# Optimization experiments

Measured on AMD Instinct MI355X. Metric: run time of the kernel, lower is better.

The kernel has to match this reference:

```python
import jax, jax.numpy as jnp
import numpy as np


def _depthwise3x3(x_nhwc, w):
    # w: (3, 3, 1, C) — depthwise conv, padding=1, matches torch Conv2d(groups=C)
    return jax.lax.conv_general_dilated(
        x_nhwc, w, window_strides=(1, 1), padding='SAME',
        dimension_numbers=('NHWC', 'HWIO', 'NHWC'),
        feature_group_count=x_nhwc.shape[-1])


def _stripe_attn(q, k, v, lepe_w, B, H, W, nh, hd, ss, axis, scale):
    # q/k/v: (B, H, W, nh*hd); axis 0 = horizontal stripes, 1 = vertical
    pad_h = (-H) % ss if axis == 0 else 0
    pad_w = (-W) % ss if axis == 1 else 0
    if pad_h or pad_w:
        pad = ((0, 0), (0, pad_h), (0, pad_w), (0, 0))
        q, k, v = jnp.pad(q, pad), jnp.pad(k, pad), jnp.pad(v, pad)
    Hp, Wp = q.shape[1], q.shape[2]
    lepe = _depthwise3x3(v, lepe_w)  # (B, Hp, Wp, nh*hd)

    if axis == 0:
        nS = Hp // ss
        def to_win(t):  # -> (B*nS*Wp, nh, ss, hd)
            t = t.reshape(B, nS, ss, Wp, nh, hd)
            return t.transpose(0, 1, 3, 4, 2, 5).reshape(B * nS * Wp, nh, ss, hd)
    else:
        nS = Wp // ss
        def to_win(t):  # -> (B*Hp*nS, nh, ss, hd)
            t = t.reshape(B, Hp, nS, ss, nh, hd)
            return t.transpose(0, 1, 2, 4, 3, 5).reshape(B * Hp * nS, nh, ss, hd)

    qw, kw, vw, lw = to_win(q), to_win(k), to_win(v), to_win(lepe)
    attn = jax.nn.softmax(jnp.einsum('wnqd,wnkd->wnqk', qw, kw) / scale, axis=-1)
    out = jnp.einsum('wnqk,wnkd->wnqd', attn, vw) + lw  # (Wnum, nh, ss, hd)

    if axis == 0:
        out = out.transpose(0, 2, 1, 3).reshape(B, nS, Wp, ss, nh * hd)
        out = out.transpose(0, 1, 3, 2, 4).reshape(B, Hp, Wp, nh * hd)
    else:
        out = out.transpose(0, 2, 1, 3).reshape(B, Hp, nS, ss, nh * hd)
        out = out.reshape(B, Hp, Wp, nh * hd)
    return out[:, :H, :W, :].reshape(B, H * W, nh * hd)


def setup_inputs() -> dict:
    key = jax.random.key(0)
    ks = jax.random.split(key, 6)
    B, H, W, dim, n_heads, ss = 8, 64, 64, 512, 16, 8
    half = dim // 2
    x = jax.random.normal(ks[0], (B, H * W, dim), dtype=jnp.float32)
    w_qkv = jax.random.normal(ks[1], (3 * dim, dim), dtype=jnp.float32) * 0.02
    w_proj = jax.random.normal(ks[2], (dim, dim), dtype=jnp.float32) * 0.02
    b_proj = jnp.zeros((dim,), dtype=jnp.float32)
    lepe_h_w = jax.random.normal(ks[3], (3, 3, 1, half), dtype=jnp.float32) * 0.1
    lepe_v_w = jax.random.normal(ks[4], (3, 3, 1, half), dtype=jnp.float32) * 0.1
    return {"x": x, "w_qkv": w_qkv, "w_proj": w_proj, "b_proj": b_proj,
            "lepe_h_w": lepe_h_w, "lepe_v_w": lepe_v_w, "H": H, "W": W}


def reference(x, w_qkv, w_proj, b_proj, lepe_h_w, lepe_v_w, H, W):
    B, L, C = x.shape
    n_heads, ss = 16, 8
    hd = C // n_heads
    scale = float(np.sqrt(hd))
    qkv = x @ w_qkv.T  # (B, L, 3C)
    q, k, v = jnp.split(qkv, 3, axis=-1)
    q = q.reshape(B, H, W, C)
    k = k.reshape(B, H, W, C)
    v = v.reshape(B, H, W, C)
    half = C // 2
    nh_h = n_heads // 2
    nh_v = n_heads - nh_h
    out_h = _stripe_attn(q[..., :half], k[..., :half], v[..., :half],
                         lepe_h_w, B, H, W, nh_h, hd, ss, axis=0, scale=scale)
    out_v = _stripe_attn(q[..., half:], k[..., half:], v[..., half:],
                         lepe_v_w, B, H, W, nh_v, hd, ss, axis=1, scale=scale)
    out = jnp.concatenate([out_h, out_v], axis=-1)
    return out @ w_proj.T + b_proj
```

## Files before the change

### kernel.cpp

```cpp
#include <hip/hip_runtime.h>
#include <hip/hip_bf16.h>
#include <stdint.h>

typedef _Float16 half2v __attribute__((ext_vector_type(2)));
typedef _Float16 half8v __attribute__((ext_vector_type(8)));
typedef uint32_t u32x4  __attribute__((ext_vector_type(4)));
typedef float    f32x4  __attribute__((ext_vector_type(4)));

__device__ __forceinline__ unsigned short f2h(float f) {
  _Float16 h = (_Float16)f;
  return __builtin_bit_cast(unsigned short, h);
}
__device__ __forceinline__ half2v bch2(uint32_t u) {
  return __builtin_bit_cast(half2v, u);
}
__device__ __forceinline__ uint32_t pkrtz_u32(float a, float b) {
  return __builtin_bit_cast(uint32_t, __builtin_amdgcn_cvt_pkrtz(a, b));
}

__device__ __forceinline__ int qkv_idx(int half, int b, int n, int h, int w) {
  int idx = half * 8388608 + (b * 8 + n) * 131072;
  idx += (half == 0) ? ((h >> 3) * 16384 + w * 256 + (h & 7) * 32)
                     : (h * 2048 + w * 32);
  return idx;
}

#define GLOAD_LDS16(gsrc, lbase)                                          \
  __builtin_amdgcn_global_load_lds(                                       \
      (const __attribute__((address_space(1))) uint32_t*)(gsrc),          \
      (__attribute__((address_space(3))) uint32_t*)(lbase), 16, 0, 0)

__global__ __launch_bounds__(256) void cvt_f32_f16(const float* __restrict__ in,
                                                   unsigned short* __restrict__ out,
                                                   int n4) {
  int i = blockIdx.x * 256 + threadIdx.x;
  if (i >= n4) return;
  float4 f = reinterpret_cast<const float4*>(in)[i];
  ushort4 u;
  u.x = f2h(f.x); u.y = f2h(f.y); u.z = f2h(f.z); u.w = f2h(f.w);
  reinterpret_cast<ushort4*>(out)[i] = u;
}

template<int MODE>
__global__ __launch_bounds__(512, 2) void gemm8(
    const unsigned short* __restrict__ A,
    const unsigned short* __restrict__ Bm,
    unsigned short* __restrict__ Cq,
    float* __restrict__ Cf,
    const float* __restrict__ bias,
    int M, int N)
{
  constexpr int K = 512;
  constexpr int NIT = 4;
  __shared__ unsigned short As[2][256 * 64];
  __shared__ unsigned short Bs[2][256 * 64];
  const int tid  = threadIdx.x;
  const int gn   = N >> 8;
  const int cpx  = gridDim.x >> 3;
  const int bid  = blockIdx.x;
  const int wgid = (bid & 7) * cpx + (bid >> 3);
  const int m0   = (wgid / gn) * 256;
  const int n0   = (wgid % gn) * 256;
  const int wave = tid >> 6, lane = tid & 63;
  const int wr  = wave >> 2;
  const int wcn = wave & 3;

  const int srow = tid >> 3;
  const int schk = ((tid & 7) ^ (srow & 7)) * 8;
  const size_t aSrc = (size_t)(m0 + srow) * K + schk;
  const size_t bSrc = (size_t)(n0 + srow) * K + schk;
  char* ldsA = (char*)(&As[0][0]) + (tid & ~63) * 16;
  char* ldsB = (char*)(&Bs[0][0]) + (tid & ~63) * 16;

#define STAGE_A8(b, kt)                                                     \
  do {                                                                      \
    GLOAD_LDS16(A + aSrc + (size_t)(kt) * 64,             ldsA + (b) * 32768);         \
    GLOAD_LDS16(A + aSrc + (size_t)64 * K + (kt) * 64,    ldsA + (b) * 32768 + 8192);  \
    GLOAD_LDS16(A + aSrc + (size_t)128 * K + (kt) * 64,   ldsA + (b) * 32768 + 16384); \
    GLOAD_LDS16(A + aSrc + (size_t)192 * K + (kt) * 64,   ldsA + (b) * 32768 + 24576); \
  } while (0)
#define STAGE_B8(b, kt)                                                     \
  do {                                                                      \
    GLOAD_LDS16(Bm + bSrc + (size_t)(kt) * 64,            ldsB + (b) * 32768);         \
    GLOAD_LDS16(Bm + bSrc + (size_t)64 * K + (kt) * 64,   ldsB + (b) * 32768 + 8192);  \
    GLOAD_LDS16(Bm + bSrc + (size_t)128 * K + (kt) * 64,  ldsB + (b) * 32768 + 16384); \
    GLOAD_LDS16(Bm + bSrc + (size_t)192 * K + (kt) * 64,  ldsB + (b) * 32768 + 24576); \
  } while (0)
#define BARS                                                                \
  __builtin_amdgcn_s_barrier();                                             \
  __builtin_amdgcn_sched_barrier(0)

  STAGE_A8(0, 0);
  STAGE_B8(0, 0);
  STAGE_B8(1, 1);

  f32x4 acc[8][4];
  const f32x4 zero = {0.f, 0.f, 0.f, 0.f};
  #pragma unroll
  for (int i = 0; i < 8; ++i)
    #pragma unroll
    for (int j = 0; j < 4; ++j) acc[i][j] = zero;

  const int lr  = lane & 15;
  const int kg  = lane >> 4;
  const int ck0 = kg ^ (lr & 7);

  asm volatile("s_waitcnt vmcnt(4)" ::: "memory");
  BARS;

#define LD_AF(buf, mg, ks)                                                  \
  do {                                                                      \
    const unsigned short* ap = &As[buf][0] +                                \
        (wr * 128 + (mg) * 64 + lr) * 64 + (((ks) ? (ck0 ^ 4) : ck0)) * 8;  \
    af[0] = *(const half8v*)(ap);                                           \
    af[1] = *(const half8v*)(ap + 1024);                                    \
    af[2] = *(const half8v*)(ap + 2048);                                    \
    af[3] = *(const half8v*)(ap + 3072);                                    \
  } while (0)
#define LD_BF(buf, ks)                                                      \
  do {                                                                      \
    const unsigned short* bp = &Bs[buf][0] +                                \
        (wcn * 64 + lr) * 64 + (((ks) ? (ck0 ^ 4) : ck0)) * 8;              \
    bf[0] = *(const half8v*)(bp);                                           \
    bf[1] = *(const half8v*)(bp + 1024);                                    \
    bf[2] = *(const half8v*)(bp + 2048);                                    \
    bf[3] = *(const half8v*)(bp + 3072);                                    \
  } while (0)
#define MROW(mg, i)                                                         \
  acc[(mg)*4+(i)][0] = __builtin_amdgcn_mfma_f32_16x16x32_f16(bf[0], af[i], acc[(mg)*4+(i)][0], 0, 0, 0); \
  acc[(mg)*4+(i)][1] = __builtin_amdgcn_mfma_f32_16x16x32_f16(bf[1], af[i], acc[(mg)*4+(i)][1], 0, 0, 0); \
  acc[(mg)*4+(i)][2] = __builtin_amdgcn_mfma_f32_16x16x32_f16(bf[2], af[i], acc[(mg)*4+(i)][2], 0, 0, 0); \
  acc[(mg)*4+(i)][3] = __builtin_amdgcn_mfma_f32_16x16x32_f16(bf[3], af[i], acc[(mg)*4+(i)][3], 0, 0, 0);
#define MFMA16(mg)                                                          \
  do {                                                                      \
    __builtin_amdgcn_s_setprio(1);                                          \
    MROW(mg, 0); MROW(mg, 1); MROW(mg, 2); MROW(mg, 3);                     \
    __builtin_amdgcn_s_setprio(0);                                          \
  } while (0)

  for (int it2 = 0; it2 < NIT; ++it2) {
    const bool more = (it2 + 1 < NIT);
    const int keven = 2 * it2;
    half8v af[4], bf[4];
    LD_BF(0, 0); LD_AF(0, 0, 0);
    STAGE_A8(1, keven + 1);
    BARS;
    MFMA16(0);
    BARS;
    LD_AF(0, 1, 0);
    BARS;
    MFMA16(1);
    BARS;
    LD_BF(0, 1); LD_AF(0, 0, 1);
    BARS;
    MFMA16(0);
    BARS;
    LD_AF(0, 1, 1);
    if (more) {
      STAGE_B8(0, keven + 2);
      asm volatile("s_waitcnt vmcnt(4)" ::: "memory");
    } else {
      asm volatile("s_waitcnt vmcnt(0)" ::: "memory");
    }
    BARS;
    MFMA16(1);
    BARS;
    LD_BF(1, 0); LD_AF(1, 0, 0);
    if (more) STAGE_A8(0, keven + 2);
    BARS;
    MFMA16(0);
    BARS;
    LD_AF(1, 1, 0);
    BARS;
    MFMA16(1);
    BARS;
    LD_BF(1, 1); LD_AF(1, 0, 1);
    BARS;
    MFMA16(0);
    BARS;
    LD_AF(1, 1, 1);
    if (more) {
      STAGE_B8(1, keven + 3);
      asm volatile("s_waitcnt vmcnt(4)" ::: "memory");
    }
    BARS;
    MFMA16(1);
    BARS;
  }
#undef STAGE_A8
#undef STAGE_B8
#undef LD_AF
#undef LD_BF
#undef MROW
#undef MFMA16
#undef BARS

  const int cr = (lane >> 4) * 4;
  const int cc = lane & 15;

  if constexpr (MODE == 0) {
    #pragma unroll
    for (int j = 0; j < 4; ++j) {
      const int n = n0 + wcn * 64 + j * 16 + cr;
      const float4 b4 = *reinterpret_cast<const float4*>(bias + n);
      #pragma unroll
      for (int i = 0; i < 8; ++i) {
        const int m = m0 + wr * 128 + i * 16 + cc;
        float4 r;
        r.x = acc[i][j][0] + b4.x;
        r.y = acc[i][j][1] + b4.y;
        r.z = acc[i][j][2] + b4.z;
        r.w = acc[i][j][3] + b4.w;
        *reinterpret_cast<float4*>(Cf + (size_t)m * N + n) = r;
      }
    }
  } else {
    const int mb   = m0 + wr * 128;
    const int btok = mb >> 12;
    const int hr0  = (mb >> 6) & 63;
    #pragma unroll
    for (int j = 0; j < 4; ++j) {
      const int nb    = n0 + wcn * 64 + j * 16 + cr;
      const int tq    = nb >> 9;
      const int halfc = (nb >> 8) & 1;
      const int nn    = (nb & 255) >> 5;
      const int ch4   = nb & 31;
      const int headbase = tq * 16777216 + halfc * 8388608 +
                           (btok * 8 + nn) * 131072 + ch4;
      #pragma unroll
      for (int i = 0; i < 8; ++i) {
        const int hrow = hr0 + (i >> 2);
        const int wpix = (i & 3) * 16 + cc;
        const int off = halfc ? (hrow * 2048 + wpix * 32)
                              : ((hrow >> 3) * 16384 + wpix * 256 + (hrow & 7) * 32);
        uint2 r;
        r.x = pkrtz_u32(acc[i][j][0], acc[i][j][1]);
        r.y = pkrtz_u32(acc[i][j][2], acc[i][j][3]);
        *reinterpret_cast<uint2*>(Cq + headbase + off) = r;
      }
    }
  }
}

__global__ __launch_bounds__(256) void attn_lepe(
    const unsigned short* __restrict__ qkvp,
    const unsigned short* __restrict__ wlep,
    unsigned short* __restrict__ outp)
{
  const int gw   = (int)((blockIdx.x * 256 + threadIdx.x) >> 6);
  const int lane = threadIdx.x & 63;
  const int half = gw >> 14;
  const int id   = gw & 16383;
  const int b    = id >> 11;
  const int n    = (id >> 8) & 7;
  int h0, w0;
  if (half == 0) { h0 = ((id >> 5) & 7) * 8; w0 = (id & 31) * 2; }
  else           { h0 = ((id >> 3) & 31) * 2; w0 = (id & 7) * 8; }
  const int baseA = qkv_idx(half, b, n, h0, w0);
  const int dWin  = (half == 0) ? 256 : 2048;
  const int baseB = baseA + dWin;

  const int qr = lane >> 3, kr = lane & 7;
  const unsigned short* qA = qkvp + baseA + qr * 32;
  const unsigned short* kA = qkvp + 16777216 + baseA + kr * 32;
  float sA = 0.f, sB = 0.f;
  #pragma unroll
  for (int c = 0; c < 4; ++c) {
    const u32x4 qa = *reinterpret_cast<const u32x4*>(qA + c * 8);
    const u32x4 ka = *reinterpret_cast<const u32x4*>(kA + c * 8);
    const u32x4 qb = *reinterpret_cast<const u32x4*>(qA + dWin + c * 8);
    const u32x4 kb = *reinterpret_cast<const u32x4*>(kA + dWin + c * 8);
    #pragma unroll
    for (int e = 0; e < 4; ++e) {
      sA = __builtin_amdgcn_fdot2(bch2(qa[e]), bch2(ka[e]), sA, false);
      sB = __builtin_amdgcn_fdot2(bch2(qb[e]), bch2(kb[e]), sB, false);
    }
  }
  const float scl = 0.17677669529663687f;
  const float pA = __expf(sA * scl);
  const float pB = __expf(sB * scl);
  float denA = pA, denB = pB;
  denA += __shfl_xor(denA, 1); denA += __shfl_xor(denA, 2); denA += __shfl_xor(denA, 4);
  denB += __shfl_xor(denB, 1); denB += __shfl_xor(denB, 2); denB += __shfl_xor(denB, 4);
  const float aAv = pA * __builtin_amdgcn_rcpf(denA);
  const float aBv = pB * __builtin_amdgcn_rcpf(denB);
  const uint32_t adu = pkrtz_u32(aAv, aBv);

  const int dgrp = lane & 3;
  const int win  = (lane >> 2) & 1;
  const int qr2  = lane >> 3;
  const int d0   = dgrp * 8;
  const int mybase = win ? baseB : baseA;
  const unsigned short* vwin = qkvp + 33554432 + mybase;

  half2v o01 = {0,0}, o23 = {0,0}, o45 = {0,0}, o67 = {0,0};
  #pragma unroll
  for (int k = 0; k < 8; ++k) {
    const uint32_t pairw = (uint32_t)__shfl((int)adu, qr2 * 8 + k);
    const half2v ph = bch2(pairw);
    const _Float16 av = win ? ph.y : ph.x;
    const half2v ak2 = {av, av};
    const u32x4 vv = *reinterpret_cast<const u32x4*>(vwin + k * 32 + d0);
    o01 += ak2 * bch2(vv[0]);
    o23 += ak2 * bch2(vv[1]);
    o45 += ak2 * bch2(vv[2]);
    o67 += ak2 * bch2(vv[3]);
  }

  const int hq = (half == 0) ? (h0 + qr2) : (h0 + win);
  const int wq = (half == 0) ? (w0 + win) : (w0 + qr2);
  const unsigned short* vplane = qkvp + 33554432;
  const unsigned short* wl = wlep + half * 2304 + n * 32 + d0;
  half2v l01 = {0,0}, l23 = {0,0}, l45 = {0,0}, l67 = {0,0};
  #pragma unroll
  for (int dy = -1; dy <= 1; ++dy) {
    #pragma unroll
    for (int dx = -1; dx <= 1; ++dx) {
      const int hh = hq + dy, ww = wq + dx;
      u32x4 vv = {0u, 0u, 0u, 0u};
      if ((unsigned)hh < 64u && (unsigned)ww < 64u)
        vv = *reinterpret_cast<const u32x4*>(vplane + qkv_idx(half, b, n, hh, ww) + d0);
      const u32x4 wt = *reinterpret_cast<const u32x4*>(wl + ((dy + 1) * 3 + dx + 1) * 256);
      l01 += bch2(wt[0]) * bch2(vv[0]);
      l23 += bch2(wt[1]) * bch2(vv[1]);
      l45 += bch2(wt[2]) * bch2(vv[2]);
      l67 += bch2(wt[3]) * bch2(vv[3]);
    }
  }

  const int m = b * 4096 + hq * 64 + wq;
  const int chan0 = half * 256 + n * 32;
  u32x4 r;
  r[0] = __builtin_bit_cast(uint32_t, (half2v)(o01 + l01));
  r[1] = __builtin_bit_cast(uint32_t, (half2v)(o23 + l23));
  r[2] = __builtin_bit_cast(uint32_t, (half2v)(o45 + l45));
  r[3] = __builtin_bit_cast(uint32_t, (half2v)(o67 + l67));
  *reinterpret_cast<u32x4*>(outp + (size_t)m * 512 + chan0 + d0) = r;
}

extern "C" void kernel_launch(void* const* d_in, const int* in_sizes, int n_in,
                              void* d_out, int out_size, void* d_ws, size_t ws_size,
                              hipStream_t stream) {
  const float* x      = (const float*)d_in[0];
  const float* w_qkv  = (const float*)d_in[1];
  const float* w_proj = (const float*)d_in[2];
  const float* b_proj = (const float*)d_in[3];
  const float* lepe_h = (const float*)d_in[4];
  const float* lepe_v = (const float*)d_in[5];
  float* out = (float*)d_out;

  char* ws = (char*)d_ws;
  unsigned short* qkv_p   = (unsigned short*)ws;
  unsigned short* xh      = (unsigned short*)(ws + 100663296);
  unsigned short* wqkv_h  = (unsigned short*)(ws + 134217728);
  unsigned short* wproj_h = (unsigned short*)(ws + 135790592);
  unsigned short* wlep_h  = (unsigned short*)(ws + 136314880);

  cvt_f32_f16<<<16384, 256, 0, stream>>>(x, xh, 4194304);
  cvt_f32_f16<<<768,   256, 0, stream>>>(w_qkv, wqkv_h, 196608);
  cvt_f32_f16<<<256,   256, 0, stream>>>(w_proj, wproj_h, 65536);
  cvt_f32_f16<<<3,     256, 0, stream>>>(lepe_h, wlep_h, 576);
  cvt_f32_f16<<<3,     256, 0, stream>>>(lepe_v, wlep_h + 2304, 576);

  gemm8<1><<<768, 512, 0, stream>>>(
      xh, wqkv_h, qkv_p, nullptr, nullptr, 32768, 1536);

  attn_lepe<<<8192, 256, 0, stream>>>(qkv_p, wlep_h, xh);

  gemm8<0><<<256, 512, 0, stream>>>(
      xh, wproj_h, nullptr, out, b_proj, 32768, 512);
}
```

Before: 175.6 us.

## Add smaller-tile projection GEMM and merge weight conversion launches

The final projection GEMM (M=32768, N=512) moves from the 256x256-tile gemm8 with 256 blocks to a new 128x128-tile kernel with 1024 blocks of 256 threads. The aim is better fill of the GPU's compute units, which the few large tiles left underused. The four small weight-conversion launches are also merged into one kernel to cut launch overhead. The cost is lower data reuse per tile and more global traffic for A and B.

```diff
diff --git a/kernel.cpp b/kernel.cpp
--- a/kernel.cpp
+++ b/kernel.cpp
@@ -39,6 +39,25 @@
   ushort4 u;
   u.x = f2h(f.x); u.y = f2h(f.y); u.z = f2h(f.z); u.w = f2h(f.w);
   reinterpret_cast<ushort4*>(out)[i] = u;
+}
+
+__global__ __launch_bounds__(256) void cvt_weights(
+    const float* __restrict__ wqkv, const float* __restrict__ wproj,
+    const float* __restrict__ lh,   const float* __restrict__ lv,
+    unsigned short* __restrict__ owqkv, unsigned short* __restrict__ owproj,
+    unsigned short* __restrict__ owlep)
+{
+  int i = blockIdx.x * 256 + threadIdx.x;
+  const float* src; unsigned short* dst; int off;
+  if      (i < 196608) { src = wqkv;  dst = owqkv;        off = i; }
+  else if (i < 262144) { src = wproj; dst = owproj;       off = i - 196608; }
+  else if (i < 262720) { src = lh;    dst = owlep;        off = i - 262144; }
+  else if (i < 263296) { src = lv;    dst = owlep + 2304; off = i - 262720; }
+  else return;
+  float4 f = reinterpret_cast<const float4*>(src)[off];
+  ushort4 u;
+  u.x = f2h(f.x); u.y = f2h(f.y); u.z = f2h(f.z); u.w = f2h(f.w);
+  reinterpret_cast<ushort4*>(dst)[off] = u;
 }
 
 template<int MODE>
@@ -242,6 +261,105 @@
   }
 }
 
+__global__ __launch_bounds__(256) void gemm_proj(
+    const unsigned short* __restrict__ A,
+    const unsigned short* __restrict__ B,
+    float* __restrict__ Cf,
+    const float* __restrict__ bias)
+{
+  constexpr int K = 512, N = 512;
+  __shared__ unsigned short As[2][128 * 32];
+  __shared__ unsigned short Bs[2][128 * 32];
+  const int tid  = threadIdx.x;
+  const int gn   = N >> 7;
+  const int cpx  = gridDim.x >> 3;
+  const int bid  = blockIdx.x;
+  const int wgid = (bid & 7) * cpx + (bid >> 3);
+  const int m0   = (wgid / gn) * 128;
+  const int n0   = (wgid % gn) * 128;
+  const int wave = tid >> 6, lane = tid & 63;
+  const int wr = wave >> 1, wc = wave & 1;
+  const int sr = tid >> 2;
+  const int sc = ((tid & 3) ^ ((tid >> 3) & 3)) * 8;
+  const size_t aBase0 = (size_t)(m0 + sr) * K + sc;
+  const size_t aBase1 = (size_t)(m0 + 64 + sr) * K + sc;
+  const size_t bBase0 = (size_t)(n0 + sr) * K + sc;
+  const size_t bBase1 = (size_t)(n0 + 64 + sr) * K + sc;
+  char* ldsA = (char*)(&As[0][0]) + (tid & ~63) * 16;
+  char* ldsB = (char*)(&Bs[0][0]) + (tid & ~63) * 16;
+
+#define STAGE_P(bsel, kofs)                                        \
+  do {                                                             \
+    GLOAD_LDS16(A + aBase0 + (kofs), ldsA + (bsel) * 8192);        \
+    GLOAD_LDS16(A + aBase1 + (kofs), ldsA + (bsel) * 8192 + 4096); \
+    GLOAD_LDS16(B + bBase0 + (kofs), ldsB + (bsel) * 8192);        \
+    GLOAD_LDS16(B + bBase1 + (kofs), ldsB + (bsel) * 8192 + 4096); \
+  } while (0)
+
+  STAGE_P(0, 0);
+
+  f32x4 acc[4][4];
+  const f32x4 zero = {0.f, 0.f, 0.f, 0.f};
+  #pragma unroll
+  for (int i = 0; i < 4; ++i)
+    #pragma unroll
+    for (int j = 0; j < 4; ++j) acc[i][j] = zero;
+
+  const int lr   = lane & 15;
+  const int slot = (lane >> 4) ^ ((lr >> 1) & 3);
+
+  auto compute = [&](const unsigned short* Asb, const unsigned short* Bsb) {
+    half8v af[4], bfr[4];
+    #pragma unroll
+    for (int i = 0; i < 4; ++i)
+      af[i] = *reinterpret_cast<const half8v*>(Asb + (wr * 64 + i * 16 + lr) * 32 + slot * 8);
+    #pragma unroll
+    for (int j = 0; j < 4; ++j)
+      bfr[j] = *reinterpret_cast<const half8v*>(Bsb + (wc * 64 + j * 16 + lr) * 32 + slot * 8);
+    __builtin_amdgcn_s_setprio(1);
+    #pragma unroll
+    for (int i = 0; i < 4; ++i)
+      #pragma unroll
+      for (int j = 0; j < 4; ++j)
+        acc[i][j] = __builtin_amdgcn_mfma_f32_16x16x32_f16(bfr[j], af[i], acc[i][j], 0, 0, 0);
+    __builtin_amdgcn_s_setprio(0);
+  };
+
+  const int nt = K >> 5;
+  for (int t = 0; t < nt - 1; ++t) {
+    STAGE_P((t + 1) & 1, (t + 1) * 32);
+    asm volatile("s_waitcnt vmcnt(4)" ::: "memory");
+    __builtin_amdgcn_s_barrier();
+    __builtin_amdgcn_sched_barrier(0);
+    compute(&As[t & 1][0], &Bs[t & 1][0]);
+    __builtin_amdgcn_s_barrier();
+    __builtin_amdgcn_sched_barrier(0);
+  }
+  asm volatile("s_waitcnt vmcnt(0)" ::: "memory");
+  __builtin_amdgcn_s_barrier();
+  __builtin_amdgcn_sched_barrier(0);
+  compute(&As[(nt - 1) & 1][0], &Bs[(nt - 1) & 1][0]);
+#undef STAGE_P
+
+  const int cr = (lane >> 4) * 4;
+  const int cc = lane & 15;
+  #pragma unroll
+  for (int j = 0; j < 4; ++j) {
+    const int n = n0 + wc * 64 + j * 16 + cr;
+    const float4 b4 = *reinterpret_cast<const float4*>(bias + n);
+    #pragma unroll
+    for (int i = 0; i < 4; ++i) {
+      const int m = m0 + wr * 64 + i * 16 + cc;
+      float4 r;
+      r.x = acc[i][j][0] + b4.x;
+      r.y = acc[i][j][1] + b4.y;
+      r.z = acc[i][j][2] + b4.z;
+      r.w = acc[i][j][3] + b4.w;
+      *reinterpret_cast<float4*>(Cf + (size_t)m * N + n) = r;
+    }
+  }
+}
+
 __global__ __launch_bounds__(256) void attn_lepe(
     const unsigned short* __restrict__ qkvp,
     const unsigned short* __restrict__ wlep,
@@ -357,16 +475,13 @@
   unsigned short* wlep_h  = (unsigned short*)(ws + 136314880);
 
   cvt_f32_f16<<<16384, 256, 0, stream>>>(x, xh, 4194304);
-  cvt_f32_f16<<<768,   256, 0, stream>>>(w_qkv, wqkv_h, 196608);
-  cvt_f32_f16<<<256,   256, 0, stream>>>(w_proj, wproj_h, 65536);
-  cvt_f32_f16<<<3,     256, 0, stream>>>(lepe_h, wlep_h, 576);
-  cvt_f32_f16<<<3,     256, 0, stream>>>(lepe_v, wlep_h + 2304, 576);
+  cvt_weights<<<1029, 256, 0, stream>>>(w_qkv, w_proj, lepe_h, lepe_v,
+                                        wqkv_h, wproj_h, wlep_h);
 
   gemm8<1><<<768, 512, 0, stream>>>(
       xh, wqkv_h, qkv_p, nullptr, nullptr, 32768, 1536);
 
   attn_lepe<<<8192, 256, 0, stream>>>(qkv_p, wlep_h, xh);
 
-  gemm8<0><<<256, 512, 0, stream>>>(
-      xh, wproj_h, nullptr, out, b_proj, 32768, 512);
-}
+  gemm_proj<<<1024, 256, 0, stream>>>(xh, wproj_h, out, b_proj);
+}
```

Result: no change. 173.4 us (-1.2%).
